# Optimization experiments

Hardware: AMD Instinct MI355X
Metric: run time of the kernel (lower is better)

The kernel has to match this reference:

```python
import jax, jax.numpy as jnp
import numpy as np

IN_F, OUT_F, RANK = 4096, 4096, 64
B, S = 4, 2048


def setup_inputs() -> dict:
    key = jax.random.key(0)
    k1, k2, k3 = jax.random.split(key, 3)
    x = jax.random.normal(k1, (B, S, IN_F), dtype=jnp.float32)
    # Low-rank compressed weight factors: W = U @ V^T, shape [OUT_F, IN_F]
    U = jax.random.normal(k2, (OUT_F, RANK), dtype=jnp.float32) / np.sqrt(RANK)
    V = jax.random.normal(k3, (IN_F, RANK), dtype=jnp.float32) / np.sqrt(IN_F)
    bias = jnp.zeros((OUT_F,), dtype=jnp.float32)
    return {"x": x, "U": U, "V": V, "bias": bias}


def reference(x, U, V, bias):
    # Decompress: weight = compressor.decompress(compressed_weight) -> [out, in]
    weight = jnp.einsum("or,ir->oi", U, V)  # materialized like the original
    # F.linear(x, weight, bias) = x @ weight^T + bias
    return jnp.einsum("bsi,oi->bso", x, weight) + bias
```

## Files before the change

### kernel.cpp

```cpp
#include <hip/hip_runtime.h>

#define IN_F    4096
#define OUT_F   4096
#define RANK    64
#define M_TOTAL 8192
#define M_TILE  16
#define BLOCK   512
#define NWAVES  8
#define KSPLIT  4

using short8  = __attribute__((ext_vector_type(8))) short;
using float4v = __attribute__((ext_vector_type(4))) float;

#define MFMA16(A, B, C) __builtin_amdgcn_mfma_f32_16x16x32_bf16((A), (B), (C), 0, 0, 0)

__device__ __forceinline__ void split2(float x, short& h, short& l) {
    unsigned u = __float_as_uint(x);
    unsigned t = u & 0xffff0000u;
    h = (short)(t >> 16);
    float r = x - __uint_as_float(t);
    l = (short)(__float_as_uint(r) >> 16);
}

__device__ __forceinline__ void split_f4x2(float4 a, float4 b, short8& hi, short8& lo) {
    short h0,h1,h2,h3,h4,h5,h6,h7, l0,l1,l2,l3,l4,l5,l6,l7;
    split2(a.x,h0,l0); split2(a.y,h1,l1); split2(a.z,h2,l2); split2(a.w,h3,l3);
    split2(b.x,h4,l4); split2(b.y,h5,l5); split2(b.z,h6,l6); split2(b.w,h7,l7);
    hi = (short8){h0,h1,h2,h3,h4,h5,h6,h7};
    lo = (short8){l0,l1,l2,l3,l4,l5,l6,l7};
}


__global__ void prep_uv(const float* __restrict__ V, const float* __restrict__ U,
                        unsigned short* __restrict__ vt_hi, unsigned short* __restrict__ vt_lo,
                        unsigned short* __restrict__ u_hi,  unsigned short* __restrict__ u_lo)
{
    const int b = blockIdx.x;
    const int linear = (b & 255) * 256 + threadIdx.x;
    short h[4], l[4];
    if (b < 256) {
        const int r  = linear >> 10;
        const int k0 = (linear & 1023) * 4;
        #pragma unroll
        for (int i = 0; i < 4; ++i)
            split2(V[(size_t)(k0 + i) * RANK + r], h[i], l[i]);
        const size_t o = (size_t)r * IN_F + k0;
        *(ushort4*)(vt_hi + o) = make_ushort4((unsigned short)h[0], (unsigned short)h[1],
                                              (unsigned short)h[2], (unsigned short)h[3]);
        *(ushort4*)(vt_lo + o) = make_ushort4((unsigned short)l[0], (unsigned short)l[1],
                                              (unsigned short)l[2], (unsigned short)l[3]);
    } else {
        const int idx = linear * 4;
        const float4 u4 = *(const float4*)(U + idx);
        split2(u4.x, h[0], l[0]); split2(u4.y, h[1], l[1]);
        split2(u4.z, h[2], l[2]); split2(u4.w, h[3], l[3]);
        *(ushort4*)(u_hi + idx) = make_ushort4((unsigned short)h[0], (unsigned short)h[1],
                                               (unsigned short)h[2], (unsigned short)h[3]);
        *(ushort4*)(u_lo + idx) = make_ushort4((unsigned short)l[0], (unsigned short)l[1],
                                               (unsigned short)l[2], (unsigned short)l[3]);
    }
}

__global__ __launch_bounds__(256, 2) void lowrank_xv3(
    const float* __restrict__ x,
    const unsigned short* __restrict__ vt_hi, const unsigned short* __restrict__ vt_lo,
    float* __restrict__ t_part)
{
    __shared__ float part[KSPLIT][64][RANK + 4];

    const int tid  = threadIdx.x;
    const int wv   = tid >> 6;
    const int lane = tid & 63;
    const int l15  = lane & 15;
    const int quad = lane >> 4;
    const int kq   = blockIdx.x & 3;
    const int mg   = blockIdx.x >> 2;
    const int m0   = mg * 64;
    const int kbase = kq * 1024 + wv * 256;

    float4v acc[4][4] = {};
    const float* xp[4];
    #pragma unroll
    for (int mf = 0; mf < 4; ++mf)
        xp[mf] = x + (size_t)(m0 + mf * 16 + l15) * IN_F + kbase + quad * 8;
    const unsigned short* vh = vt_hi + (size_t)l15 * IN_F + kbase + quad * 8;
    const unsigned short* vl = vt_lo + (size_t)l15 * IN_F + kbase + quad * 8;

    #pragma unroll
    for (int ks = 0; ks < 8; ++ks) {
        const int k0 = ks * 32;
        float4 xa[4], xb[4];
        #pragma unroll
        for (int mf = 0; mf < 4; ++mf) {
            xa[mf] = *(const float4*)(xp[mf] + k0);
            xb[mf] = *(const float4*)(xp[mf] + k0 + 4);
        }
        short8 bh[4], bl[4];
        #pragma unroll
        for (int rt = 0; rt < 4; ++rt) {
            bh[rt] = *(const short8*)(vh + (size_t)rt * 16 * IN_F + k0);
            bl[rt] = *(const short8*)(vl + (size_t)rt * 16 * IN_F + k0);
        }
        #pragma unroll
        for (int mf = 0; mf < 4; ++mf) {
            short8 a_hi, a_lo;
            split_f4x2(xa[mf], xb[mf], a_hi, a_lo);
            #pragma unroll
            for (int rt = 0; rt < 4; ++rt) {
                acc[mf][rt] = MFMA16(a_lo, bh[rt], acc[mf][rt]);
                acc[mf][rt] = MFMA16(a_hi, bl[rt], acc[mf][rt]);
                acc[mf][rt] = MFMA16(a_hi, bh[rt], acc[mf][rt]);
            }
        }
    }

    #pragma unroll
    for (int mf = 0; mf < 4; ++mf)
        #pragma unroll
        for (int rt = 0; rt < 4; ++rt)
            #pragma unroll
            for (int rg = 0; rg < 4; ++rg)
                part[wv][mf * 16 + quad * 4 + rg][rt * 16 + l15] = acc[mf][rt][rg];
    __syncthreads();

    {
        const int e  = tid * 16;
        const int m  = e >> 6;
        const int r0 = e & 63;
        float* dst = t_part + (size_t)kq * (M_TOTAL * RANK)
                   + (size_t)(m0 + m) * RANK + r0;
        #pragma unroll
        for (int j = 0; j < 4; ++j) {
            float4 s = {0.f, 0.f, 0.f, 0.f};
            #pragma unroll
            for (int p = 0; p < KSPLIT; ++p) {
                const float4 v = *(const float4*)(&part[p][m][r0 + j * 4]);
                s.x += v.x; s.y += v.y; s.z += v.z; s.w += v.w;
            }
            *(float4*)(dst + j * 4) = s;
        }
    }
}

__global__ void reduce_t(const float* __restrict__ t_part,
                         unsigned short* __restrict__ t_hi, unsigned short* __restrict__ t_lo)
{
    const size_t e = (size_t)(blockIdx.x * 256 + threadIdx.x) * 4;
    float4 s = *(const float4*)(t_part + e);
    #pragma unroll
    for (int p = 1; p < KSPLIT; ++p) {
        const float4 a = *(const float4*)(t_part + (size_t)p * (M_TOTAL * RANK) + e);
        s.x += a.x; s.y += a.y; s.z += a.z; s.w += a.w;
    }
    short h[4], l[4];
    split2(s.x, h[0], l[0]); split2(s.y, h[1], l[1]);
    split2(s.z, h[2], l[2]); split2(s.w, h[3], l[3]);
    *(ushort4*)(t_hi + e) = make_ushort4((unsigned short)h[0], (unsigned short)h[1],
                                         (unsigned short)h[2], (unsigned short)h[3]);
    *(ushort4*)(t_lo + e) = make_ushort4((unsigned short)l[0], (unsigned short)l[1],
                                         (unsigned short)l[2], (unsigned short)l[3]);
}

__global__ __launch_bounds__(256, 3) void lowrank_tu3(
    const unsigned short* __restrict__ t_hi, const unsigned short* __restrict__ t_lo,
    const unsigned short* __restrict__ u_hi, const unsigned short* __restrict__ u_lo,
    const float* __restrict__ bias, float* __restrict__ out)
{
    const int tid  = threadIdx.x;
    const int wv   = tid >> 6;
    const int lane = tid & 63;
    const int l15  = lane & 15;
    const int quad = lane >> 4;
    const int og   = blockIdx.x & 31;
    const int mg   = blockIdx.x >> 5;
    const int m0   = mg * 256 + wv * 64;
    const int o0   = og * 128;

    short8 ta_hi[4][2], ta_lo[4][2];
    #pragma unroll
    for (int mf = 0; mf < 4; ++mf) {
        const unsigned short* tp_h = t_hi + (size_t)(m0 + mf * 16 + l15) * RANK + quad * 8;
        const unsigned short* tp_l = t_lo + (size_t)(m0 + mf * 16 + l15) * RANK + quad * 8;
        ta_hi[mf][0] = *(const short8*)(tp_h);   ta_hi[mf][1] = *(const short8*)(tp_h + 32);
        ta_lo[mf][0] = *(const short8*)(tp_l);   ta_lo[mf][1] = *(const short8*)(tp_l + 32);
    }

    const unsigned short* up_h = u_hi + (size_t)(o0 + l15) * RANK + quad * 8;
    const unsigned short* up_l = u_lo + (size_t)(o0 + l15) * RANK + quad * 8;
    short8 uh0 = *(const short8*)(up_h), uh1 = *(const short8*)(up_h + 32);
    short8 ul0 = *(const short8*)(up_l), ul1 = *(const short8*)(up_l + 32);

    #pragma unroll
    for (int nt = 0; nt < 8; ++nt) {
        short8 nh0 = uh0, nh1 = uh1, nl0 = ul0, nl1 = ul1;
        if (nt < 7) {
            const int adv = (nt + 1) * 16 * RANK;
            nh0 = *(const short8*)(up_h + adv);   nh1 = *(const short8*)(up_h + adv + 32);
            nl0 = *(const short8*)(up_l + adv);   nl1 = *(const short8*)(up_l + adv + 32);
        }
        const int o = o0 + nt * 16 + l15;
        const float bv = bias[o];
        #pragma unroll
        for (int mf = 0; mf < 4; ++mf) {
            float4v acc = {bv, bv, bv, bv};
            acc = MFMA16(ta_lo[mf][0], uh0, acc);
            acc = MFMA16(ta_hi[mf][0], ul0, acc);
            acc = MFMA16(ta_hi[mf][0], uh0, acc);
            acc = MFMA16(ta_lo[mf][1], uh1, acc);
            acc = MFMA16(ta_hi[mf][1], ul1, acc);
            acc = MFMA16(ta_hi[mf][1], uh1, acc);
            float* op = out + (size_t)(m0 + mf * 16 + quad * 4) * OUT_F + o;
            op[0 * OUT_F] = acc[0];
            op[1 * OUT_F] = acc[1];
            op[2 * OUT_F] = acc[2];
            op[3 * OUT_F] = acc[3];
        }
        uh0 = nh0; uh1 = nh1; ul0 = nl0; ul1 = nl1;
    }
}


__global__ __launch_bounds__(BLOCK, 4) void lowrank_xv(
    const float* __restrict__ x,
    const unsigned short* __restrict__ vt_hi, const unsigned short* __restrict__ vt_lo,
    unsigned short* __restrict__ t_hi, unsigned short* __restrict__ t_lo)
{
    __shared__ float part[NWAVES][M_TILE][RANK + 4];

    const int tid  = threadIdx.x;
    const int wv   = tid >> 6;
    const int lane = tid & 63;
    const int l15  = lane & 15;
    const int quad = lane >> 4;
    const int m0   = blockIdx.x * M_TILE;

    float4v acc[4] = {};
    const float*          xp = x     + (size_t)(m0 + l15) * IN_F + wv * 512 + quad * 8;
    const unsigned short* vh = vt_hi + (size_t)l15 * IN_F + wv * 512 + quad * 8;
    const unsigned short* vl = vt_lo + (size_t)l15 * IN_F + wv * 512 + quad * 8;

    float4 xa = *(const float4*)(xp);
    float4 xb = *(const float4*)(xp + 4);
    #pragma unroll
    for (int ks = 0; ks < 16; ++ks) {
        const int k0 = ks * 32;
        float4 na = xa, nb = xb;
        if (ks < 15) {
            na = *(const float4*)(xp + k0 + 32);
            nb = *(const float4*)(xp + k0 + 36);
        }
        short8 a_hi, a_lo;
        split_f4x2(xa, xb, a_hi, a_lo);
        #pragma unroll
        for (int rt = 0; rt < 4; ++rt) {
            short8 b_hi = *(const short8*)(vh + (size_t)rt * 16 * IN_F + k0);
            short8 b_lo = *(const short8*)(vl + (size_t)rt * 16 * IN_F + k0);
            acc[rt] = MFMA16(a_lo, b_hi, acc[rt]);
            acc[rt] = MFMA16(a_hi, b_lo, acc[rt]);
            acc[rt] = MFMA16(a_hi, b_hi, acc[rt]);
        }
        xa = na; xb = nb;
    }

    #pragma unroll
    for (int rt = 0; rt < 4; ++rt)
        #pragma unroll
        for (int rg = 0; rg < 4; ++rg)
            part[wv][quad * 4 + rg][rt * 16 + l15] = acc[rt][rg];
    __syncthreads();

    const int e = tid * 2;
    const int m = e >> 6, r = e & 63;
    float s0 = 0.f, s1 = 0.f;
    #pragma unroll
    for (int w = 0; w < NWAVES; ++w) { s0 += part[w][m][r]; s1 += part[w][m][r + 1]; }
    short h0, l0, h1, l1;
    split2(s0, h0, l0); split2(s1, h1, l1);
    const size_t off = (size_t)m0 * RANK + e;
    *(ushort2*)(t_hi + off) = make_ushort2((unsigned short)h0, (unsigned short)h1);
    *(ushort2*)(t_lo + off) = make_ushort2((unsigned short)l0, (unsigned short)l1);
}

__global__ __launch_bounds__(256, 4) void lowrank_tu(
    const unsigned short* __restrict__ t_hi, const unsigned short* __restrict__ t_lo,
    const unsigned short* __restrict__ u_hi, const unsigned short* __restrict__ u_lo,
    const float* __restrict__ bias, float* __restrict__ out)
{
    const int tid  = threadIdx.x;
    const int wv   = tid >> 6;
    const int lane = tid & 63;
    const int l15  = lane & 15;
    const int quad = lane >> 4;
    const int og   = blockIdx.x & 7;
    const int mg   = blockIdx.x >> 3;
    const int m0   = mg * 64 + wv * 16;
    const int o0   = og * 512;

    short8 ta_hi[2], ta_lo[2];
    {
        const unsigned short* tp_h = t_hi + (size_t)(m0 + l15) * RANK + quad * 8;
        const unsigned short* tp_l = t_lo + (size_t)(m0 + l15) * RANK + quad * 8;
        ta_hi[0] = *(const short8*)(tp_h);   ta_hi[1] = *(const short8*)(tp_h + 32);
        ta_lo[0] = *(const short8*)(tp_l);   ta_lo[1] = *(const short8*)(tp_l + 32);
    }

    #pragma unroll 2
    for (int nt = 0; nt < 32; ++nt) {
        const int o = o0 + nt * 16 + l15;
        const unsigned short* up_h = u_hi + (size_t)o * RANK + quad * 8;
        const unsigned short* up_l = u_lo + (size_t)o * RANK + quad * 8;
        const float bv = bias[o];
        float4v acc = {bv, bv, bv, bv};
        #pragma unroll
        for (int ks = 0; ks < 2; ++ks) {
            short8 uh = *(const short8*)(up_h + ks * 32);
            short8 ul = *(const short8*)(up_l + ks * 32);
            acc = MFMA16(ta_lo[ks], uh, acc);
            acc = MFMA16(ta_hi[ks], ul, acc);
            acc = MFMA16(ta_hi[ks], uh, acc);
        }
        float* op = out + (size_t)(m0 + quad * 4) * OUT_F + o;
        op[0 * OUT_F] = acc[0];
        op[1 * OUT_F] = acc[1];
        op[2 * OUT_F] = acc[2];
        op[3 * OUT_F] = acc[3];
    }
}

__global__ __launch_bounds__(256, 2) void fallback_fp32(
    const float* __restrict__ x, const float* __restrict__ U,
    const float* __restrict__ V, const float* __restrict__ bias,
    float* __restrict__ out)
{
    __shared__ float v_lds[128][RANK];
    __shared__ float t_lds[8][RANK];
    const int tid = threadIdx.x, lane = tid & 63, wave = tid >> 6;
    const int m0 = blockIdx.x * 8;
    float acc0 = 0.f, acc1 = 0.f;
    const size_t row_base = (size_t)(m0 + wave * 2) * IN_F;
    for (int kt = 0; kt < IN_F; kt += 128) {
        const float4* Vg = (const float4*)(V + (size_t)kt * RANK);
        float4* Vs = (float4*)(&v_lds[0][0]);
        #pragma unroll
        for (int i = 0; i < 8; ++i) Vs[tid + 256 * i] = Vg[tid + 256 * i];
        __syncthreads();
        const float* xp = x + row_base + kt;
        #pragma unroll 8
        for (int k = 0; k < 128; k += 4) {
            float v0 = v_lds[k+0][lane], v1 = v_lds[k+1][lane];
            float v2 = v_lds[k+2][lane], v3 = v_lds[k+3][lane];
            float4 xa = *(const float4*)(xp + 0 * IN_F + k);
            float4 xb = *(const float4*)(xp + 1 * IN_F + k);
            acc0 += xa.x*v0 + xa.y*v1 + xa.z*v2 + xa.w*v3;
            acc1 += xb.x*v0 + xb.y*v1 + xb.z*v2 + xb.w*v3;
        }
        __syncthreads();
    }
    t_lds[wave*2+0][lane] = acc0;
    t_lds[wave*2+1][lane] = acc1;
    __syncthreads();
    for (int oc = 0; oc < OUT_F; oc += 1024) {
        const int o4 = oc + tid * 4;
        const float4 b4 = *(const float4*)(bias + o4);
        float4 a0=b4,a1=b4,a2=b4,a3=b4,a4=b4,a5=b4,a6=b4,a7=b4;
        const float* Up = U + (size_t)o4 * RANK;
        #pragma unroll 2
        for (int r0 = 0; r0 < RANK; r0 += 4) {
            const float4 u0 = *(const float4*)(Up + 0*RANK + r0);
            const float4 u1 = *(const float4*)(Up + 1*RANK + r0);
            const float4 u2 = *(const float4*)(Up + 2*RANK + r0);
            const float4 u3 = *(const float4*)(Up + 3*RANK + r0);
            #define P2_STEP(AM, MM) { \
                const float4 t4 = *(const float4*)(&t_lds[MM][r0]); \
                AM.x += t4.x*u0.x + t4.y*u0.y + t4.z*u0.z + t4.w*u0.w; \
                AM.y += t4.x*u1.x + t4.y*u1.y + t4.z*u1.z + t4.w*u1.w; \
                AM.z += t4.x*u2.x + t4.y*u2.y + t4.z*u2.z + t4.w*u2.w; \
                AM.w += t4.x*u3.x + t4.y*u3.y + t4.z*u3.z + t4.w*u3.w; }
            P2_STEP(a0,0) P2_STEP(a1,1) P2_STEP(a2,2) P2_STEP(a3,3)
            P2_STEP(a4,4) P2_STEP(a5,5) P2_STEP(a6,6) P2_STEP(a7,7)
            #undef P2_STEP
        }
        float* op = out + (size_t)m0 * OUT_F + o4;
        *(float4*)(op+0*OUT_F)=a0; *(float4*)(op+1*OUT_F)=a1;
        *(float4*)(op+2*OUT_F)=a2; *(float4*)(op+3*OUT_F)=a3;
        *(float4*)(op+4*OUT_F)=a4; *(float4*)(op+5*OUT_F)=a5;
        *(float4*)(op+6*OUT_F)=a6; *(float4*)(op+7*OUT_F)=a7;
    }
}

extern "C" void kernel_launch(void* const* d_in, const int* in_sizes, int n_in,
                              void* d_out, int out_size, void* d_ws, size_t ws_size,
                              hipStream_t stream) {
    const float* x    = (const float*)d_in[0];
    const float* U    = (const float*)d_in[1];
    const float* V    = (const float*)d_in[2];
    const float* bias = (const float*)d_in[3];
    float* out = (float*)d_out;

    const size_t E = (size_t)RANK * IN_F;
    const size_t T = (size_t)M_TOTAL * RANK;
    const size_t need_v4 = (E * 4 + T * 2) * sizeof(unsigned short)
                         + (size_t)KSPLIT * T * sizeof(float);
    const size_t need_v2 = (E * 4 + T * 2) * sizeof(unsigned short);

    if (ws_size >= need_v4) {
        unsigned short* vt_hi = (unsigned short*)d_ws;
        unsigned short* vt_lo = vt_hi + E;
        unsigned short* u_hi  = vt_lo + E;
        unsigned short* u_lo  = u_hi  + E;
        unsigned short* t_hi  = u_lo  + E;
        unsigned short* t_lo  = t_hi  + T;
        float*          t_part = (float*)(t_lo + T);
        prep_uv<<<dim3(512), dim3(256), 0, stream>>>(V, U, vt_hi, vt_lo, u_hi, u_lo);
        lowrank_xv3<<<dim3((M_TOTAL / 64) * KSPLIT), dim3(256), 0, stream>>>(
            x, vt_hi, vt_lo, t_part);
        reduce_t<<<dim3(T / (256 * 4)), dim3(256), 0, stream>>>(t_part, t_hi, t_lo);
        lowrank_tu3<<<dim3((M_TOTAL / 256) * (OUT_F / 128)), dim3(256), 0, stream>>>(
            t_hi, t_lo, u_hi, u_lo, bias, out);
    } else if (ws_size >= need_v2) {
        unsigned short* vt_hi = (unsigned short*)d_ws;
        unsigned short* vt_lo = vt_hi + E;
        unsigned short* u_hi  = vt_lo + E;
        unsigned short* u_lo  = u_hi  + E;
        unsigned short* t_hi  = u_lo  + E;
        unsigned short* t_lo  = t_hi  + T;
        prep_uv<<<dim3(512), dim3(256), 0, stream>>>(V, U, vt_hi, vt_lo, u_hi, u_lo);
        lowrank_xv<<<dim3(M_TOTAL / M_TILE), dim3(BLOCK), 0, stream>>>(
            x, vt_hi, vt_lo, t_hi, t_lo);
        lowrank_tu<<<dim3((M_TOTAL / 64) * (OUT_F / 512)), dim3(256), 0, stream>>>(
            t_hi, t_lo, u_hi, u_lo, bias, out);
    } else {
        fallback_fp32<<<dim3(M_TOTAL / 8), dim3(256), 0, stream>>>(x, U, V, bias, out);
    }
}
```

Baseline: 298.1 us.

## Fuse split-K reduction into output GEMM and prefetch next K-step in xV kernel

Removes the separate reduce_t kernel. The output kernel now sums the four fp32 split-K partials of T directly and splits them into bf16 hi/lo in registers. The x·V kernel also double-buffers its global loads, issuing the next K-step's x and V^T fragments before the current MFMAs to hide load latency. The cost is that each output block re-reads the fp32 partials (32 blocks share each row group), and the prefetch buffers raise register pressure.

```diff
diff --git a/kernel.cpp b/kernel.cpp
--- a/kernel.cpp
+++ b/kernel.cpp
@@ -61,7 +61,7 @@
     }
 }
 
-__global__ __launch_bounds__(256, 2) void lowrank_xv3(
+__global__ __launch_bounds__(256, 2) void lowrank_xv4(
     const float* __restrict__ x,
     const unsigned short* __restrict__ vt_hi, const unsigned short* __restrict__ vt_lo,
     float* __restrict__ t_part)
@@ -86,20 +86,39 @@
     const unsigned short* vh = vt_hi + (size_t)l15 * IN_F + kbase + quad * 8;
     const unsigned short* vl = vt_lo + (size_t)l15 * IN_F + kbase + quad * 8;
 
+    float4 xa[4], xb[4];
+    short8 bh[4], bl[4];
+    #pragma unroll
+    for (int mf = 0; mf < 4; ++mf) {
+        xa[mf] = *(const float4*)(xp[mf]);
+        xb[mf] = *(const float4*)(xp[mf] + 4);
+    }
+    #pragma unroll
+    for (int rt = 0; rt < 4; ++rt) {
+        bh[rt] = *(const short8*)(vh + (size_t)rt * 16 * IN_F);
+        bl[rt] = *(const short8*)(vl + (size_t)rt * 16 * IN_F);
+    }
+
     #pragma unroll
     for (int ks = 0; ks < 8; ++ks) {
-        const int k0 = ks * 32;
-        float4 xa[4], xb[4];
+        const int kn = (ks + 1) * 32;
+        float4 na[4], nb[4];
+        short8 nh[4], nl[4];
         #pragma unroll
         for (int mf = 0; mf < 4; ++mf) {
-            xa[mf] = *(const float4*)(xp[mf] + k0);
-            xb[mf] = *(const float4*)(xp[mf] + k0 + 4);
-        }
-        short8 bh[4], bl[4];
+            na[mf] = xa[mf]; nb[mf] = xb[mf];
+            if (ks < 7) {
+                na[mf] = *(const float4*)(xp[mf] + kn);
+                nb[mf] = *(const float4*)(xp[mf] + kn + 4);
+            }
+        }
         #pragma unroll
         for (int rt = 0; rt < 4; ++rt) {
-            bh[rt] = *(const short8*)(vh + (size_t)rt * 16 * IN_F + k0);
-            bl[rt] = *(const short8*)(vl + (size_t)rt * 16 * IN_F + k0);
+            nh[rt] = bh[rt]; nl[rt] = bl[rt];
+            if (ks < 7) {
+                nh[rt] = *(const short8*)(vh + (size_t)rt * 16 * IN_F + kn);
+                nl[rt] = *(const short8*)(vl + (size_t)rt * 16 * IN_F + kn);
+            }
         }
         #pragma unroll
         for (int mf = 0; mf < 4; ++mf) {
@@ -112,6 +131,10 @@
                 acc[mf][rt] = MFMA16(a_hi, bh[rt], acc[mf][rt]);
             }
         }
+        #pragma unroll
+        for (int mf = 0; mf < 4; ++mf) { xa[mf] = na[mf]; xb[mf] = nb[mf]; }
+        #pragma unroll
+        for (int rt = 0; rt < 4; ++rt) { bh[rt] = nh[rt]; bl[rt] = nl[rt]; }
     }
 
     #pragma unroll
@@ -142,27 +165,8 @@
     }
 }
 
-__global__ void reduce_t(const float* __restrict__ t_part,
-                         unsigned short* __restrict__ t_hi, unsigned short* __restrict__ t_lo)
-{
-    const size_t e = (size_t)(blockIdx.x * 256 + threadIdx.x) * 4;
-    float4 s = *(const float4*)(t_part + e);
-    #pragma unroll
-    for (int p = 1; p < KSPLIT; ++p) {
-        const float4 a = *(const float4*)(t_part + (size_t)p * (M_TOTAL * RANK) + e);
-        s.x += a.x; s.y += a.y; s.z += a.z; s.w += a.w;
-    }
-    short h[4], l[4];
-    split2(s.x, h[0], l[0]); split2(s.y, h[1], l[1]);
-    split2(s.z, h[2], l[2]); split2(s.w, h[3], l[3]);
-    *(ushort4*)(t_hi + e) = make_ushort4((unsigned short)h[0], (unsigned short)h[1],
-                                         (unsigned short)h[2], (unsigned short)h[3]);
-    *(ushort4*)(t_lo + e) = make_ushort4((unsigned short)l[0], (unsigned short)l[1],
-                                         (unsigned short)l[2], (unsigned short)l[3]);
-}
-
-__global__ __launch_bounds__(256, 3) void lowrank_tu3(
-    const unsigned short* __restrict__ t_hi, const unsigned short* __restrict__ t_lo,
+__global__ __launch_bounds__(256, 3) void lowrank_tu4(
+    const float* __restrict__ t_part,
     const unsigned short* __restrict__ u_hi, const unsigned short* __restrict__ u_lo,
     const float* __restrict__ bias, float* __restrict__ out)
 {
@@ -179,10 +183,25 @@
     short8 ta_hi[4][2], ta_lo[4][2];
     #pragma unroll
     for (int mf = 0; mf < 4; ++mf) {
-        const unsigned short* tp_h = t_hi + (size_t)(m0 + mf * 16 + l15) * RANK + quad * 8;
-        const unsigned short* tp_l = t_lo + (size_t)(m0 + mf * 16 + l15) * RANK + quad * 8;
-        ta_hi[mf][0] = *(const short8*)(tp_h);   ta_hi[mf][1] = *(const short8*)(tp_h + 32);
-        ta_lo[mf][0] = *(const short8*)(tp_l);   ta_lo[mf][1] = *(const short8*)(tp_l + 32);
+        const float* tp = t_part + (size_t)(m0 + mf * 16 + l15) * RANK + quad * 8;
+        float4 s0 = *(const float4*)(tp);
+        float4 s1 = *(const float4*)(tp + 4);
+        float4 s2 = *(const float4*)(tp + 32);
+        float4 s3 = *(const float4*)(tp + 36);
+        #pragma unroll
+        for (int p = 1; p < KSPLIT; ++p) {
+            const float* q = tp + (size_t)p * (M_TOTAL * RANK);
+            const float4 a0 = *(const float4*)(q);
+            const float4 a1 = *(const float4*)(q + 4);
+            const float4 a2 = *(const float4*)(q + 32);
+            const float4 a3 = *(const float4*)(q + 36);
+            s0.x += a0.x; s0.y += a0.y; s0.z += a0.z; s0.w += a0.w;
+            s1.x += a1.x; s1.y += a1.y; s1.z += a1.z; s1.w += a1.w;
+            s2.x += a2.x; s2.y += a2.y; s2.z += a2.z; s2.w += a2.w;
+            s3.x += a3.x; s3.y += a3.y; s3.z += a3.z; s3.w += a3.w;
+        }
+        split_f4x2(s0, s1, ta_hi[mf][0], ta_lo[mf][0]);
+        split_f4x2(s2, s3, ta_hi[mf][1], ta_lo[mf][1]);
     }
 
     const unsigned short* up_h = u_hi + (size_t)(o0 + l15) * RANK + quad * 8;
@@ -399,24 +418,21 @@
 
     const size_t E = (size_t)RANK * IN_F;
     const size_t T = (size_t)M_TOTAL * RANK;
-    const size_t need_v4 = (E * 4 + T * 2) * sizeof(unsigned short)
+    const size_t need_v5 = (E * 4) * sizeof(unsigned short)
                          + (size_t)KSPLIT * T * sizeof(float);
     const size_t need_v2 = (E * 4 + T * 2) * sizeof(unsigned short);
 
-    if (ws_size >= need_v4) {
+    if (ws_size >= need_v5) {
         unsigned short* vt_hi = (unsigned short*)d_ws;
         unsigned short* vt_lo = vt_hi + E;
         unsigned short* u_hi  = vt_lo + E;
         unsigned short* u_lo  = u_hi  + E;
-        unsigned short* t_hi  = u_lo  + E;
-        unsigned short* t_lo  = t_hi  + T;
-        float*          t_part = (float*)(t_lo + T);
+        float*          t_part = (float*)(u_lo + E);
         prep_uv<<<dim3(512), dim3(256), 0, stream>>>(V, U, vt_hi, vt_lo, u_hi, u_lo);
-        lowrank_xv3<<<dim3((M_TOTAL / 64) * KSPLIT), dim3(256), 0, stream>>>(
+        lowrank_xv4<<<dim3((M_TOTAL / 64) * KSPLIT), dim3(256), 0, stream>>>(
             x, vt_hi, vt_lo, t_part);
-        reduce_t<<<dim3(T / (256 * 4)), dim3(256), 0, stream>>>(t_part, t_hi, t_lo);
-        lowrank_tu3<<<dim3((M_TOTAL / 256) * (OUT_F / 128)), dim3(256), 0, stream>>>(
-            t_hi, t_lo, u_hi, u_lo, bias, out);
+        lowrank_tu4<<<dim3((M_TOTAL / 256) * (OUT_F / 128)), dim3(256), 0, stream>>>(
+            t_part, u_hi, u_lo, bias, out);
     } else if (ws_size >= need_v2) {
         unsigned short* vt_hi = (unsigned short*)d_ws;
         unsigned short* vt_lo = vt_hi + E;
```

Measured after the change: 320.8 us. 7.6% more time.
